# Kernel optimization log

Hardware: AMD Instinct MI355X
Metric: run time of the kernel (lower is better)

Reference implementation:

```python
import jax, jax.numpy as jnp
import numpy as np

C = 512
NUM_GROUPS = 32
EPS = 1e-6


def setup_inputs() -> dict:
    key = jax.random.key(0)
    ks = jax.random.split(key, 10)
    x = jax.random.normal(ks[0], (2, C, 64, 64), dtype=jnp.float32)
    s = 1.0 / np.sqrt(C)
    return {
        "x": x,
        "gn_gamma": jnp.ones((C,), jnp.float32),
        "gn_beta": jnp.zeros((C,), jnp.float32),
        "wq": jax.random.normal(ks[1], (C, C), jnp.float32) * s,
        "bq": jnp.zeros((C,), jnp.float32),
        "wk": jax.random.normal(ks[2], (C, C), jnp.float32) * s,
        "bk": jnp.zeros((C,), jnp.float32),
        "wv": jax.random.normal(ks[3], (C, C), jnp.float32) * s,
        "bv": jnp.zeros((C,), jnp.float32),
        "wo": jax.random.normal(ks[4], (C, C), jnp.float32) * s,
        "bo": jnp.zeros((C,), jnp.float32),
    }


def group_norm(x, gamma, beta):
    b, c, h, w = x.shape
    xg = x.reshape(b, NUM_GROUPS, c // NUM_GROUPS, h, w)
    mean = xg.mean(axis=(2, 3, 4), keepdims=True)
    var = xg.var(axis=(2, 3, 4), keepdims=True)
    xg = (xg - mean) * jax.lax.rsqrt(var + EPS)
    x = xg.reshape(b, c, h, w)
    return x * gamma[None, :, None, None] + beta[None, :, None, None]


def conv1x1(x, w, bias):
    # 1x1 conv == channel matmul: (b,c,h,w),(o,c) -> (b,o,h,w)
    return jnp.einsum('bchw,oc->bohw', x, w) + bias[None, :, None, None]


def reference(x, gn_gamma, gn_beta, wq, bq, wk, bk, wv, bv, wo, bo):
    b, c, h, w = x.shape
    hn = group_norm(x, gn_gamma, gn_beta)
    q = conv1x1(hn, wq, bq).reshape(b, c, h * w)  # (b,c,n)
    k = conv1x1(hn, wk, bk).reshape(b, c, h * w)
    v = conv1x1(hn, wv, bv).reshape(b, c, h * w)
    scale = int(c) ** (-0.5)
    # scores[b,i,j] = sum_c q[b,c,i] k[b,c,j]
    scores = jnp.einsum('bci,bcj->bij', q, k) * scale
    attn = jax.nn.softmax(scores, axis=2)
    out = jnp.einsum('bcj,bij->bci', v, attn).reshape(b, c, h, w)
    out = conv1x1(out, wo, bo)
    return x + out
```

## Files before the change

### kernel.cpp

```cpp
#include <hip/hip_runtime.h>

typedef unsigned short ushort_t;
typedef unsigned char uchar_t;
typedef __bf16 bf16x8 __attribute__((ext_vector_type(8)));
typedef float f32x4 __attribute__((ext_vector_type(4)));

__device__ __forceinline__ ushort_t f2bf(float f) {
  unsigned u = __float_as_uint(f);
  u += 0x7fff + ((u >> 16) & 1);
  return (ushort_t)(u >> 16);
}

__device__ __forceinline__ void gload16(const void* g, void* l) {
  __builtin_amdgcn_global_load_lds(
      (const __attribute__((address_space(1))) unsigned int*)g,
      (__attribute__((address_space(3))) unsigned int*)l, 16, 0, 0);
}

__global__ __launch_bounds__(256) void cvt_weights(
    const float* __restrict__ wq, const float* __restrict__ wk,
    const float* __restrict__ wv, const float* __restrict__ wo,
    const float* __restrict__ bq, const float* __restrict__ bk,
    ushort_t* __restrict__ dst, float* __restrict__ qkbias,
    float* __restrict__ stats2) {
  int b = blockIdx.x, t = threadIdx.x;
  if (b < 1024) {
    int i = b * 256 + t;
    dst[i]          = f2bf(wq[i]);
    dst[262144 + i] = f2bf(wk[i]);
    dst[524288 + i] = f2bf(wv[i]);
    dst[786432 + i] = f2bf(wo[i]);
  } else if (b < 1028) {
    int j = (b - 1024) * 256 + t;
    qkbias[j] = (j < 512) ? bq[j] : bk[j - 512];
  } else {
    if (t < 128) stats2[t] = 0.f;
  }
}

__global__ __launch_bounds__(256) void zero_f32(float* __restrict__ p) {
  p[blockIdx.x * 256 + threadIdx.x] = 0.f;
}

__global__ __launch_bounds__(256) void gn_stats_partial(const float* __restrict__ x,
                                                        float* __restrict__ stats2) {
  int bg = blockIdx.x >> 2, q = blockIdx.x & 3;
  const float4* p = (const float4*)(x + (size_t)bg * 65536 + q * 16384);
  float s = 0.f, ss = 0.f;
  for (int i = threadIdx.x; i < 4096; i += 256) {
    float4 v = p[i];
    s += v.x + v.y + v.z + v.w;
    ss += v.x * v.x + v.y * v.y + v.z * v.z + v.w * v.w;
  }
  for (int off = 32; off; off >>= 1) {
    s += __shfl_xor(s, off, 64);
    ss += __shfl_xor(ss, off, 64);
  }
  __shared__ float sh[8];
  int wave = threadIdx.x >> 6, lane = threadIdx.x & 63;
  if (lane == 0) { sh[wave] = s; sh[4 + wave] = ss; }
  __syncthreads();
  if (threadIdx.x == 0) {
    atomicAdd(&stats2[bg * 2], sh[0] + sh[1] + sh[2] + sh[3]);
    atomicAdd(&stats2[bg * 2 + 1], sh[4] + sh[5] + sh[6] + sh[7]);
  }
}

__global__ __launch_bounds__(64) void gn_finalize(const float* __restrict__ stats2,
                                                  float* __restrict__ stats) {
  int t = threadIdx.x;
  float s = stats2[t * 2], ss = stats2[t * 2 + 1];
  float mean = s * (1.f / 65536.f);
  float var = ss * (1.f / 65536.f) - mean * mean;
  stats[t * 2] = mean;
  stats[t * 2 + 1] = rsqrtf(var + 1e-6f);
}

__global__ __launch_bounds__(256) void gn_apply(
    const float* __restrict__ x, const float* __restrict__ gamma,
    const float* __restrict__ beta, const float* __restrict__ stats,
    ushort_t* __restrict__ hnT) {
  __shared__ float T[32][33];
  int i0 = blockIdx.x * 32, c0 = blockIdx.y * 32, b = blockIdx.z;
  int tx = threadIdx.x, ty = threadIdx.y;
#pragma unroll
  for (int k = 0; k < 4; k++) {
    int cl = ty + k * 8;
    int c = c0 + cl;
    int bg = (b * 32 + (c >> 4)) * 2;
    float mean = stats[bg], rstd = stats[bg + 1];
    float v = x[((size_t)(b * 512 + c)) * 4096 + i0 + tx];
    T[cl][tx] = (v - mean) * rstd * gamma[c] + beta[c];
  }
  __syncthreads();
#pragma unroll
  for (int k = 0; k < 4; k++) {
    int il = ty + k * 8;
    hnT[((size_t)b * 4096 + i0 + il) * 512 + c0 + tx] = f2bf(T[tx][il]);
  }
}

template <int BN, int UNR>
__global__ __launch_bounds__(256) void gemm_abt(
    const ushort_t* __restrict__ A, long long sA, int lda,
    const ushort_t* __restrict__ B, long long sB, int ldb,
    int K, int N, int ldc,
    ushort_t* __restrict__ outB, long long sC,
    const float* __restrict__ bias, int bias_mode, float scale,
    float* __restrict__ outF, const float* __restrict__ resid,
    float* __restrict__ rowsum, const float* __restrict__ colscale,
    int swiz, int omode) {
  constexpr int CPW = (8 + BN / 16) / 4;
  constexpr int SB = (128 + BN) * 32;
  constexpr int STEP = 32 * UNR;
  constexpr int MI = (BN == 128) ? 4 : 2;
  constexpr int NI = 4;
  __shared__ __align__(16) ushort_t Ls[2][UNR * SB];

  int bx = blockIdx.x, by = blockIdx.y, bz = blockIdx.z;
  if (swiz) {
    unsigned nx = gridDim.x, ny = gridDim.y;
    unsigned id = (blockIdx.z * ny + blockIdx.y) * nx + blockIdx.x;
    unsigned pb8 = (nx * ny) >> 3;
    unsigned c = id & 7, j = id >> 3;
    bz = j / pb8;
    unsigned jb = j - bz * pb8;
    unsigned jy = jb / nx;
    by = c * (ny >> 3) + jy;
    bx = jb - jy * nx;
  }

  int m0 = by * 128, n0 = bx * BN;
  int t = threadIdx.x;
  int lane = t & 63;
  int quad = lane >> 4, l16 = lane & 15;
  int wave = t >> 6;
  int wm = (BN == 128) ? (wave >> 1) * 64 : wave * 32;
  int wn = (BN == 128) ? (wave & 1) * 64 : 0;

  f32x4 acc[MI][NI];
#pragma unroll
  for (int i = 0; i < MI; i++)
#pragma unroll
    for (int j = 0; j < NI; j++)
#pragma unroll
      for (int r = 0; r < 4; r++) acc[i][j][r] = 0.f;

  const ushort_t* gp[CPW];
  int lofs[CPW];
  int crow = lane >> 2, skoff = (lane & 3) * 8;
#pragma unroll
  for (int i = 0; i < CPW; i++) {
    int c = wave * CPW + i;
    if (c < 8) {
      gp[i] = A + (size_t)bz * sA + (size_t)(m0 + c * 16 + crow) * lda + skoff;
      lofs[i] = c * 1024 + lane * 16;
    } else {
      int slot = (c - 8) * 16 + crow;
      int arow = (slot & ~63) + ((slot & 15) * 4) + ((slot & 63) >> 4);
      gp[i] = B + (size_t)bz * sB + (size_t)(n0 + arow) * ldb + skoff;
      lofs[i] = 8192 + (c - 8) * 1024 + lane * 16;
    }
  }
  char* lbase = (char*)&Ls[0][0];

#pragma unroll
  for (int s = 0; s < UNR; s++)
#pragma unroll
    for (int i = 0; i < CPW; i++)
      gload16(gp[i] + s * 32, lbase + s * (SB * 2) + lofs[i]);

  for (int k0 = 0; k0 < K; k0 += STEP) {
    int p = (k0 / STEP) & 1;
    __syncthreads();
    if (k0 + STEP < K) {
      int pofs = (p ^ 1) * (UNR * SB * 2);
#pragma unroll
      for (int s = 0; s < UNR; s++)
#pragma unroll
        for (int i = 0; i < CPW; i++)
          gload16(gp[i] + k0 + STEP + s * 32, lbase + pofs + s * (SB * 2) + lofs[i]);
    }
#pragma unroll
    for (int s = 0; s < UNR; s++) {
      bf16x8 af[MI], bfr[NI];
#pragma unroll
      for (int i = 0; i < MI; i++)
        af[i] = *(const bf16x8*)&Ls[p][s * SB + (wm + i * 16 + l16) * 32 + quad * 8];
#pragma unroll
      for (int j = 0; j < NI; j++)
        bfr[j] = *(const bf16x8*)&Ls[p][s * SB + 4096 + (wn + j * 16 + l16) * 32 + quad * 8];
#pragma unroll
      for (int mi = 0; mi < MI; mi++)
#pragma unroll
        for (int ni = 0; ni < NI; ni++)
          acc[mi][ni] = __builtin_amdgcn_mfma_f32_16x16x32_bf16(af[mi], bfr[ni], acc[mi][ni], 0, 0, 0);
    }
  }

  size_t cbase = (size_t)bz * sC;
  int gnb = n0 + wn + l16 * 4;
  float cs4[4] = {1.f, 1.f, 1.f, 1.f};
  if (colscale) {
    float4 c4 = *(const float4*)&colscale[(size_t)bz * N + gnb];
    cs4[0] = 1.f / c4.x; cs4[1] = 1.f / c4.y; cs4[2] = 1.f / c4.z; cs4[3] = 1.f / c4.w;
  }
  float b4[4] = {0.f, 0.f, 0.f, 0.f};
  if (bias_mode == 2) {
    float4 t4 = *(const float4*)&bias[gnb];
    b4[0] = t4.x; b4[1] = t4.y; b4[2] = t4.z; b4[3] = t4.w;
  }
#pragma unroll
  for (int mi = 0; mi < MI; mi++) {
#pragma unroll
    for (int r = 0; r < 4; r++) {
      int m = m0 + wm + mi * 16 + quad * 4 + r;
      float rbias = (bias_mode == 1) ? bias[m] : 0.f;
      float v4[4];
      float rs = 0.f;
#pragma unroll
      for (int ni = 0; ni < NI; ni++) {
        float val = acc[mi][ni][r];
        if (colscale) val *= cs4[ni];
        val += (bias_mode == 2) ? b4[ni] : rbias;
        val *= scale;
        if (rowsum) { val = __expf(val) * 0.0625f; rs += val; }
        v4[ni] = val;
      }
      size_t idx = cbase + (size_t)m * ldc + gnb;
      if (omode == 1) {
        float4 rv = *(const float4*)&resid[idx];
        float4 ov = make_float4(v4[0] + rv.x, v4[1] + rv.y, v4[2] + rv.z, v4[3] + rv.w);
        *(float4*)&outF[idx] = ov;
      } else if (omode == 2) {
        unsigned w = __builtin_amdgcn_cvt_pk_fp8_f32(v4[0], v4[1], 0u, false);
        w = __builtin_amdgcn_cvt_pk_fp8_f32(v4[2], v4[3], w, true);
        *(unsigned*)&((uchar_t*)outB)[idx] = w;
      } else {
        unsigned lo = (unsigned)f2bf(v4[0]) | ((unsigned)f2bf(v4[1]) << 16);
        unsigned hi = (unsigned)f2bf(v4[2]) | ((unsigned)f2bf(v4[3]) << 16);
        *(uint2*)&outB[idx] = make_uint2(lo, hi);
      }
      if (rowsum) {
        rs += __shfl_xor(rs, 1, 64);
        rs += __shfl_xor(rs, 2, 64);
        rs += __shfl_xor(rs, 4, 64);
        rs += __shfl_xor(rs, 8, 64);
        if (l16 == 0) atomicAdd(&rowsum[(size_t)bz * 4096 + m], rs);
      }
    }
  }
}

template <int BN, int BKB>
__global__ __launch_bounds__(256) void gemm_fp8(
    const uchar_t* __restrict__ A, long long sA, int lda,
    const uchar_t* __restrict__ B, long long sB, int ldb,
    int K, int ldc,
    void* __restrict__ outp, long long sC,
    float scale, float* __restrict__ rowsum, int swiz, int omode) {
  constexpr int SBB = (128 + BN) * BKB;
  constexpr int BASEB = 128 * BKB;
  constexpr int CPW = (8 + BN / 16) / 4;
  constexpr int NP = SBB / 4096;
  constexpr int NL = (BKB == 64) ? CPW : NP;
  constexpr int MI = (BN == 128) ? 4 : 2;
  constexpr int NI = 4;
  __shared__ __align__(16) uchar_t Ls[2][SBB];

  int bx = blockIdx.x, by = blockIdx.y, bz = blockIdx.z;
  if (swiz) {
    unsigned nx = gridDim.x, ny = gridDim.y;
    unsigned id = (blockIdx.z * ny + blockIdx.y) * nx + blockIdx.x;
    unsigned pb8 = (nx * ny) >> 3;
    unsigned c = id & 7, j = id >> 3;
    bz = j / pb8;
    unsigned jb = j - bz * pb8;
    unsigned jy = jb / nx;
    by = c * (ny >> 3) + jy;
    bx = jb - jy * nx;
  }

  int m0 = by * 128, n0 = bx * BN;
  int t = threadIdx.x;
  int lane = t & 63;
  int quad = lane >> 4, l16 = lane & 15;
  int wave = t >> 6;
  int wm = (BN == 128) ? (wave >> 1) * 64 : wave * 32;
  int wn = (BN == 128) ? (wave & 1) * 64 : 0;

  f32x4 acc[MI][NI];
#pragma unroll
  for (int i = 0; i < MI; i++)
#pragma unroll
    for (int j = 0; j < NI; j++)
#pragma unroll
      for (int r = 0; r < 4; r++) acc[i][j][r] = 0.f;

  const uchar_t* gp[NL];
  int lofs[NL];
  if constexpr (BKB == 64) {
    int r16 = lane & 15, sseg = quad * 16;
#pragma unroll
    for (int i = 0; i < NL; i++) {
      int c = wave * CPW + i;
      if (c < 8) {
        gp[i] = A + (size_t)bz * sA + (size_t)(m0 + c * 16 + r16) * lda + sseg;
        lofs[i] = c * 1024 + lane * 16;
      } else {
        int slot = (c - 8) * 16 + r16;
        int arow = (slot & ~63) + ((slot & 15) * 4) + ((slot & 63) >> 4);
        gp[i] = B + (size_t)bz * sB + (size_t)(n0 + arow) * ldb + sseg;
        lofs[i] = BASEB + (c - 8) * 1024 + lane * 16;
      }
    }
  } else {
#pragma unroll
    for (int i = 0; i < NL; i++) {
      int o = i * 4096 + t * 16;
      int row = o >> 7;
      int kb = (o & 127) ^ ((row & 7) << 4);
      if (row < 128) {
        gp[i] = A + (size_t)bz * sA + (size_t)(m0 + row) * lda + kb;
      } else {
        int br = row - 128;
        int g = br & ~63, loc = br & 63;
        int ar = g + (loc & 15) * 4 + (loc >> 4);
        gp[i] = B + (size_t)bz * sB + (size_t)(n0 + ar) * ldb + kb;
      }
      lofs[i] = o;
    }
  }
  char* lbase = (char*)&Ls[0][0];

#pragma unroll
  for (int i = 0; i < NL; i++) gload16(gp[i], lbase + lofs[i]);

  for (int k0 = 0; k0 < K; k0 += BKB) {
    int p = (k0 / BKB) & 1;
    __syncthreads();
    if (k0 + BKB < K) {
      int pofs = (p ^ 1) * SBB;
#pragma unroll
      for (int i = 0; i < NL; i++)
        gload16(gp[i] + k0 + BKB, lbase + pofs + lofs[i]);
    }
    const uchar_t* Lp = &Ls[p][0];
    if constexpr (BKB == 64) {
      int vbase = l16 * 16 + (quad >> 1) * 256 + (quad & 1) * 8;
      long long af[2][MI], bfv[2][NI];
#pragma unroll
      for (int s = 0; s < 2; s++) {
#pragma unroll
        for (int i = 0; i < MI; i++)
          af[s][i] = *(const long long*)&Lp[wm * 64 + i * 1024 + s * 512 + vbase];
#pragma unroll
        for (int j = 0; j < NI; j++)
          bfv[s][j] = *(const long long*)&Lp[BASEB + wn * 64 + j * 1024 + s * 512 + vbase];
      }
#pragma unroll
      for (int s = 0; s < 2; s++)
#pragma unroll
        for (int mi = 0; mi < MI; mi++)
#pragma unroll
          for (int ni = 0; ni < NI; ni++)
            acc[mi][ni] = __builtin_amdgcn_mfma_f32_16x16x32_fp8_fp8(af[s][mi], bfv[s][ni], acc[mi][ni], 0, 0, 0);
    } else {
      int swz = (l16 & 7) << 4;
#pragma unroll
      for (int ks = 0; ks < 4; ks++) {
        int kx = (ks * 32 + quad * 8) ^ swz;
        long long af[MI], bfv[NI];
#pragma unroll
        for (int i = 0; i < MI; i++)
          af[i] = *(const long long*)&Lp[(wm + i * 16 + l16) * 128 + kx];
#pragma unroll
        for (int j = 0; j < NI; j++)
          bfv[j] = *(const long long*)&Lp[BASEB + (wn + j * 16 + l16) * 128 + kx];
#pragma unroll
        for (int mi = 0; mi < MI; mi++)
#pragma unroll
          for (int ni = 0; ni < NI; ni++)
            acc[mi][ni] = __builtin_amdgcn_mfma_f32_16x16x32_fp8_fp8(af[mi], bfv[ni], acc[mi][ni], 0, 0, 0);
      }
    }
  }

  size_t cbase = (size_t)bz * sC;
  int gnb = n0 + wn + l16 * 4;
#pragma unroll
  for (int mi = 0; mi < MI; mi++) {
#pragma unroll
    for (int r = 0; r < 4; r++) {
      int m = m0 + wm + mi * 16 + quad * 4 + r;
      if (omode == 2) {
        float v4[4];
        float rs = 0.f;
#pragma unroll
        for (int ni = 0; ni < NI; ni++) {
          v4[ni] = __expf(acc[mi][ni][r] * scale) * 0.0625f;
          rs += v4[ni];
        }
        unsigned w = __builtin_amdgcn_cvt_pk_fp8_f32(v4[0], v4[1], 0u, false);
        w = __builtin_amdgcn_cvt_pk_fp8_f32(v4[2], v4[3], w, true);
        *(unsigned*)&((uchar_t*)outp)[cbase + (size_t)m * ldc + gnb] = w;
        rs += __shfl_xor(rs, 1, 64);
        rs += __shfl_xor(rs, 2, 64);
        rs += __shfl_xor(rs, 4, 64);
        rs += __shfl_xor(rs, 8, 64);
        if (l16 == 0) atomicAdd(&rowsum[(size_t)bz * 4096 + m], rs);
      } else {
        unsigned lo = (unsigned)f2bf(acc[mi][0][r]) | ((unsigned)f2bf(acc[mi][1][r]) << 16);
        unsigned hi = (unsigned)f2bf(acc[mi][2][r]) | ((unsigned)f2bf(acc[mi][3][r]) << 16);
        *(uint2*)&((ushort_t*)outp)[cbase + (size_t)m * ldc + gnb] = make_uint2(lo, hi);
      }
    }
  }
}

extern "C" void kernel_launch(void* const* d_in, const int* in_sizes, int n_in,
                              void* d_out, int out_size, void* d_ws, size_t ws_size,
                              hipStream_t stream) {
  const float* x     = (const float*)d_in[0];
  const float* gamma = (const float*)d_in[1];
  const float* beta  = (const float*)d_in[2];
  const float* wq    = (const float*)d_in[3];
  const float* bq    = (const float*)d_in[4];
  const float* wk    = (const float*)d_in[5];
  const float* bk    = (const float*)d_in[6];
  const float* wv    = (const float*)d_in[7];
  const float* bv    = (const float*)d_in[8];
  const float* wo    = (const float*)d_in[9];
  const float* bo    = (const float*)d_in[10];
  float* out = (float*)d_out;

  ushort_t* wb  = (ushort_t*)d_ws;
  ushort_t* wvb = wb + 524288;
  ushort_t* wob = wb + 786432;
  ushort_t* hnT = wb + 1048576;
  uchar_t*  qk8 = (uchar_t*)(hnT + 4194304);
  uchar_t*  vC8 = qk8 + 8388608;
  ushort_t* OT  = (ushort_t*)(vC8 + 4194304);
  uchar_t*  S8  = (uchar_t*)(OT + 4194304);
  float* fbuf   = (float*)(S8 + 33554432);
  float* stats  = fbuf;
  float* stats2 = fbuf + 128;
  float* qkbias = fbuf + 256;
  float* l      = (float*)hnT;

  const long long HS = 2097152;
  const long long QS = 4194304;
  const long long SS = 16777216;
  const float scale = 0.044194173824159216f;

  cvt_weights<<<dim3(1029), dim3(256), 0, stream>>>(wq, wk, wv, wo, bq, bk, wb, qkbias, stats2);
  gn_stats_partial<<<dim3(256), dim3(256), 0, stream>>>(x, stats2);
  gn_finalize<<<dim3(1), dim3(64), 0, stream>>>(stats2, stats);
  gn_apply<<<dim3(128, 16, 2), dim3(32, 8), 0, stream>>>(x, gamma, beta, stats, hnT);
  gemm_abt<128, 2><<<dim3(8, 32, 2), dim3(256), 0, stream>>>(
      hnT, HS, 512, wb, 0, 512, 512, 1024, 1024, (ushort_t*)qk8, QS, qkbias, 2, 1.f,
      nullptr, nullptr, nullptr, nullptr, 1, 2);
  gemm_abt<64, 2><<<dim3(64, 4, 2), dim3(256), 0, stream>>>(
      wvb, 0, 512, hnT, HS, 512, 512, 4096, 4096, (ushort_t*)vC8, HS, bv, 1, 1.f,
      nullptr, nullptr, nullptr, nullptr, 0, 2);
  zero_f32<<<dim3(32), dim3(256), 0, stream>>>(l);
  gemm_fp8<128, 128><<<dim3(32, 32, 2), dim3(256), 0, stream>>>(
      qk8, QS, 1024, qk8 + 512, QS, 1024, 512, 4096, S8, SS, scale, l, 1, 2);
  gemm_fp8<64, 128><<<dim3(8, 32, 2), dim3(256), 0, stream>>>(
      S8, SS, 4096, vC8, HS, 4096, 4096, 512, OT, HS, 1.f, nullptr, 1, 0);
  gemm_abt<64, 2><<<dim3(64, 4, 2), dim3(256), 0, stream>>>(
      wob, 0, 512, OT, HS, 512, 512, 4096, 4096, nullptr, HS, bo, 1, 1.f,
      out, x, nullptr, l, 0, 1);
}
```

Measured before the change: 231.2 us.

## Prefetch two K-tiles ahead in fp8 GEMM with explicit vmcnt waits

The fp8 GEMM drops the unused BKB=64 path and restructures its main loop. Loads now run two K-tiles ahead, gated by explicit s_waitcnt vmcnt counts instead of a __syncthreads at the top of every iteration. Compute sections are wrapped in s_setprio, and the next buffer's refill is issued after a second barrier once LDS reads finish. The aim is to hide global-to-LDS latency behind MFMA work, at the cost of fragile hand-tuned wait counts that must match the number of loads each thread issues.

```diff
diff --git a/kernel.cpp b/kernel.cpp
--- a/kernel.cpp
+++ b/kernel.cpp
@@ -252,18 +252,16 @@
   }
 }
 
-template <int BN, int BKB>
+template <int BN>
 __global__ __launch_bounds__(256) void gemm_fp8(
     const uchar_t* __restrict__ A, long long sA, int lda,
     const uchar_t* __restrict__ B, long long sB, int ldb,
     int K, int ldc,
     void* __restrict__ outp, long long sC,
     float scale, float* __restrict__ rowsum, int swiz, int omode) {
-  constexpr int SBB = (128 + BN) * BKB;
-  constexpr int BASEB = 128 * BKB;
-  constexpr int CPW = (8 + BN / 16) / 4;
-  constexpr int NP = SBB / 4096;
-  constexpr int NL = (BKB == 64) ? CPW : NP;
+  constexpr int SBB = (128 + BN) * 128;
+  constexpr int BASEB = 128 * 128;
+  constexpr int NL = SBB / 4096;
   constexpr int MI = (BN == 128) ? 4 : 2;
   constexpr int NI = 4;
   __shared__ __align__(16) uchar_t Ls[2][SBB];
@@ -299,90 +297,68 @@
 
   const uchar_t* gp[NL];
   int lofs[NL];
-  if constexpr (BKB == 64) {
-    int r16 = lane & 15, sseg = quad * 16;
-#pragma unroll
-    for (int i = 0; i < NL; i++) {
-      int c = wave * CPW + i;
-      if (c < 8) {
-        gp[i] = A + (size_t)bz * sA + (size_t)(m0 + c * 16 + r16) * lda + sseg;
-        lofs[i] = c * 1024 + lane * 16;
-      } else {
-        int slot = (c - 8) * 16 + r16;
-        int arow = (slot & ~63) + ((slot & 15) * 4) + ((slot & 63) >> 4);
-        gp[i] = B + (size_t)bz * sB + (size_t)(n0 + arow) * ldb + sseg;
-        lofs[i] = BASEB + (c - 8) * 1024 + lane * 16;
-      }
-    }
-  } else {
-#pragma unroll
-    for (int i = 0; i < NL; i++) {
-      int o = i * 4096 + t * 16;
-      int row = o >> 7;
-      int kb = (o & 127) ^ ((row & 7) << 4);
-      if (row < 128) {
-        gp[i] = A + (size_t)bz * sA + (size_t)(m0 + row) * lda + kb;
-      } else {
-        int br = row - 128;
-        int g = br & ~63, loc = br & 63;
-        int ar = g + (loc & 15) * 4 + (loc >> 4);
-        gp[i] = B + (size_t)bz * sB + (size_t)(n0 + ar) * ldb + kb;
-      }
-      lofs[i] = o;
-    }
+#pragma unroll
+  for (int i = 0; i < NL; i++) {
+    int o = i * 4096 + t * 16;
+    int row = o >> 7;
+    int kb = (o & 127) ^ ((row & 7) << 4);
+    if (row < 128) {
+      gp[i] = A + (size_t)bz * sA + (size_t)(m0 + row) * lda + kb;
+    } else {
+      int br = row - 128;
+      int g = br & ~63, loc = br & 63;
+      int ar = g + (loc & 15) * 4 + (loc >> 4);
+      gp[i] = B + (size_t)bz * sB + (size_t)(n0 + ar) * ldb + kb;
+    }
+    lofs[i] = o;
   }
   char* lbase = (char*)&Ls[0][0];
 
+  const int NT = K >> 7;
 #pragma unroll
   for (int i = 0; i < NL; i++) gload16(gp[i], lbase + lofs[i]);
-
-  for (int k0 = 0; k0 < K; k0 += BKB) {
-    int p = (k0 / BKB) & 1;
-    __syncthreads();
-    if (k0 + BKB < K) {
-      int pofs = (p ^ 1) * SBB;
+#pragma unroll
+  for (int i = 0; i < NL; i++) gload16(gp[i] + 128, lbase + SBB + lofs[i]);
+
+  int swz = (l16 & 7) << 4;
+  for (int kt = 0; kt < NT; ++kt) {
+    if (kt < NT - 1) {
+      if constexpr (BN == 128)
+        asm volatile("s_waitcnt vmcnt(8)" ::: "memory");
+      else
+        asm volatile("s_waitcnt vmcnt(6)" ::: "memory");
+    } else {
+      asm volatile("s_waitcnt vmcnt(0)" ::: "memory");
+    }
+    __builtin_amdgcn_s_barrier();
+    const uchar_t* Lp = &Ls[kt & 1][0];
+    __builtin_amdgcn_s_setprio(1);
+#pragma unroll
+    for (int ks = 0; ks < 4; ks++) {
+      int kx = (ks * 32 + quad * 8) ^ swz;
+      long long af[MI], bfv[NI];
+#pragma unroll
+      for (int i = 0; i < MI; i++)
+        af[i] = *(const long long*)&Lp[(wm + i * 16 + l16) * 128 + kx];
+#pragma unroll
+      for (int j = 0; j < NI; j++)
+        bfv[j] = *(const long long*)&Lp[BASEB + (wn + j * 16 + l16) * 128 + kx];
+#pragma unroll
+      for (int mi = 0; mi < MI; mi++)
+#pragma unroll
+        for (int ni = 0; ni < NI; ni++)
+          acc[mi][ni] = __builtin_amdgcn_mfma_f32_16x16x32_fp8_fp8(af[mi], bfv[ni], acc[mi][ni], 0, 0, 0);
+    }
+    __builtin_amdgcn_s_setprio(0);
+    if (kt + 2 < NT) {
+      asm volatile("s_waitcnt lgkmcnt(0)" ::: "memory");
+      __builtin_amdgcn_sched_barrier(0);
+      __builtin_amdgcn_s_barrier();
+      int pofs = (kt & 1) * SBB;
+      int ko = (kt + 2) * 128;
 #pragma unroll
       for (int i = 0; i < NL; i++)
-        gload16(gp[i] + k0 + BKB, lbase + pofs + lofs[i]);
-    }
-    const uchar_t* Lp = &Ls[p][0];
-    if constexpr (BKB == 64) {
-      int vbase = l16 * 16 + (quad >> 1) * 256 + (quad & 1) * 8;
-      long long af[2][MI], bfv[2][NI];
-#pragma unroll
-      for (int s = 0; s < 2; s++) {
-#pragma unroll
-        for (int i = 0; i < MI; i++)
-          af[s][i] = *(const long long*)&Lp[wm * 64 + i * 1024 + s * 512 + vbase];
-#pragma unroll
-        for (int j = 0; j < NI; j++)
-          bfv[s][j] = *(const long long*)&Lp[BASEB + wn * 64 + j * 1024 + s * 512 + vbase];
-      }
-#pragma unroll
-      for (int s = 0; s < 2; s++)
-#pragma unroll
-        for (int mi = 0; mi < MI; mi++)
-#pragma unroll
-          for (int ni = 0; ni < NI; ni++)
-            acc[mi][ni] = __builtin_amdgcn_mfma_f32_16x16x32_fp8_fp8(af[s][mi], bfv[s][ni], acc[mi][ni], 0, 0, 0);
-    } else {
-      int swz = (l16 & 7) << 4;
-#pragma unroll
-      for (int ks = 0; ks < 4; ks++) {
-        int kx = (ks * 32 + quad * 8) ^ swz;
-        long long af[MI], bfv[NI];
-#pragma unroll
-        for (int i = 0; i < MI; i++)
-          af[i] = *(const long long*)&Lp[(wm + i * 16 + l16) * 128 + kx];
-#pragma unroll
-        for (int j = 0; j < NI; j++)
-          bfv[j] = *(const long long*)&Lp[BASEB + (wn + j * 16 + l16) * 128 + kx];
-#pragma unroll
-        for (int mi = 0; mi < MI; mi++)
-#pragma unroll
-          for (int ni = 0; ni < NI; ni++)
-            acc[mi][ni] = __builtin_amdgcn_mfma_f32_16x16x32_fp8_fp8(af[mi], bfv[ni], acc[mi][ni], 0, 0, 0);
-      }
+        gload16(gp[i] + ko, lbase + pofs + lofs[i]);
     }
   }
 
@@ -464,9 +440,9 @@
       wvb, 0, 512, hnT, HS, 512, 512, 4096, 4096, (ushort_t*)vC8, HS, bv, 1, 1.f,
       nullptr, nullptr, nullptr, nullptr, 0, 2);
   zero_f32<<<dim3(32), dim3(256), 0, stream>>>(l);
-  gemm_fp8<128, 128><<<dim3(32, 32, 2), dim3(256), 0, stream>>>(
+  gemm_fp8<128><<<dim3(32, 32, 2), dim3(256), 0, stream>>>(
       qk8, QS, 1024, qk8 + 512, QS, 1024, 512, 4096, S8, SS, scale, l, 1, 2);
-  gemm_fp8<64, 128><<<dim3(8, 32, 2), dim3(256), 0, stream>>>(
+  gemm_fp8<64><<<dim3(8, 32, 2), dim3(256), 0, stream>>>(
       S8, SS, 4096, vC8, HS, 4096, 4096, 512, OT, HS, 1.f, nullptr, 1, 0);
   gemm_abt<64, 2><<<dim3(64, 4, 2), dim3(256), 0, stream>>>(
       wob, 0, 512, OT, HS, 512, 512, 4096, 4096, nullptr, HS, bo, 1, 1.f,
```

After: 231.5 us. Within noise of the previous version (+0.1%).
